# Kernel optimization log

Measured on AMD Instinct MI355X. Metric: run time of the kernel, lower is better.

## Reference

```python
import jax, jax.numpy as jnp
import numpy as np

DIM = 192
R = 16            # patches_resolution, D=H=W=R
SP = 4            # split_size
NH = 6            # num_heads (block level); per-branch heads = NH//3
B = 2
L = R * R * R
EPS = 1e-5


def layernorm(x, g, b):
    mu = jnp.mean(x, axis=-1, keepdims=True)
    var = jnp.mean(jnp.square(x - mu), axis=-1, keepdims=True)
    return (x - mu) * jax.lax.rsqrt(var + EPS) * g + b


def window_partition(x, d_sp, h_sp, w_sp, nh):
    b, _, _, _, cb = x.shape
    win = d_sp * h_sp * w_sp
    x = x.reshape(b, R // d_sp, d_sp, R // h_sp, h_sp, R // w_sp, w_sp, cb)
    x = x.transpose(0, 1, 3, 5, 2, 4, 6, 7).reshape(-1, win, nh, cb // nh)
    return x.transpose(0, 2, 1, 3)


def window_merge(x, d_sp, h_sp, w_sp, b):
    cb = x.shape[-1]
    x = x.reshape(b, R // d_sp, R // h_sp, R // w_sp, d_sp, h_sp, w_sp, cb)
    x = x.transpose(0, 1, 4, 2, 5, 3, 6, 7).reshape(b, L, cb)
    return x


def lepe_attention(q, k, v, d_sp, h_sp, w_sp, nh):
    # q,k,v: (B, L, Cb). Note: LePE bias is computed-but-unused in the source -> pure windowed SDPA.
    b, _, cb = q.shape
    hd = cb // nh
    scale = hd ** -0.5
    q5 = q.reshape(b, R, R, R, cb)
    k5 = k.reshape(b, R, R, R, cb)
    v5 = v.reshape(b, R, R, R, cb)
    qw = window_partition(q5, d_sp, h_sp, w_sp, nh) * scale
    kw = window_partition(k5, d_sp, h_sp, w_sp, nh)
    vw = window_partition(v5, d_sp, h_sp, w_sp, nh)
    attn = jax.nn.softmax(jnp.einsum('whqd,whkd->whqk', qw, kw), axis=-1)
    out = jnp.einsum('whqk,whkd->whqd', attn, vw)
    out = out.transpose(0, 2, 1, 3).reshape(-1, d_sp * h_sp * w_sp, cb)
    return window_merge(out, d_sp, h_sp, w_sp, b)


WINDOW_SHAPES = [(R, R, SP), (R, SP, R), (SP, R, R)]  # idx 0,1,2


def setup_inputs() -> dict:
    key = jax.random.key(0)
    ks = jax.random.split(key, 12)
    C = DIM
    H4 = int(C * 4)
    inp = {
        'x': jax.random.normal(ks[0], (B, C, R, R, R), dtype=jnp.float32),
        'w_qkv': jax.random.normal(ks[1], (C, 3 * C), dtype=jnp.float32) * (C ** -0.5),
        'w_proj': jax.random.normal(ks[2], (C, C), dtype=jnp.float32) * (C ** -0.5),
        'b_proj': jnp.zeros((C,), dtype=jnp.float32),
        'g1': jnp.ones((C,), dtype=jnp.float32),
        'b1': jnp.zeros((C,), dtype=jnp.float32),
        'g2': jnp.ones((C,), dtype=jnp.float32),
        'b2': jnp.zeros((C,), dtype=jnp.float32),
        'w_fc1': jax.random.normal(ks[3], (C, H4), dtype=jnp.float32) * (C ** -0.5),
        'b_fc1': jnp.zeros((H4,), dtype=jnp.float32),
        'w_fc2': jax.random.normal(ks[4], (H4, C), dtype=jnp.float32) * (H4 ** -0.5),
        'b_fc2': jnp.zeros((C,), dtype=jnp.float32),
    }
    return inp


def reference(x, w_qkv, w_proj, b_proj, g1, b1, g2, b2, w_fc1, b_fc1, w_fc2, b_fc2):
    C = DIM
    Cb = C // 3
    nh_b = NH // 3
    x = 2.0 * x
    xt = jnp.transpose(x, (0, 2, 3, 4, 1))                # (B, D, H, W, C)
    img = layernorm(xt, g1, b1)
    qkv = img.reshape(B, L, C) @ w_qkv                    # (B, L, 3C)
    q, k, v = jnp.split(qkv.reshape(B, L, 3, C).transpose(2, 0, 1, 3), 3, axis=0)
    q, k, v = q[0], k[0], v[0]                            # each (B, L, C)
    outs = []
    for i, (dsp, hsp, wsp) in enumerate(WINDOW_SHAPES):
        sl = slice(i * Cb, (i + 1) * Cb)
        outs.append(lepe_attention(q[..., sl], k[..., sl], v[..., sl], dsp, hsp, wsp, nh_b))
    attened = jnp.concatenate(outs, axis=2)               # (B, L, C)
    attened = attened @ w_proj + b_proj
    xs = xt.reshape(B, L, C) + attened
    h = layernorm(xs, g2, b2) @ w_fc1 + b_fc1
    h = jax.nn.gelu(h, approximate=False)
    xs = xs + (h @ w_fc2 + b_fc2)
    out = xs.reshape(B, R, R, R, C).transpose(0, 4, 1, 2, 3)  # (B, C, D, H, W)
    return out
```

## Files before the change

kernel.cpp:

```cpp
#include <hip/hip_runtime.h>
#include <hip/hip_bf16.h>

typedef __hip_bfloat16 bf16;
typedef short short8 __attribute__((ext_vector_type(8)));
typedef float floatx4 __attribute__((ext_vector_type(4)));

#define SZ (8192*192)

__device__ __forceinline__ unsigned short f2b(float f) {
    unsigned u = __builtin_bit_cast(unsigned, f);
    u += 0x7FFFu + ((u >> 16) & 1u);
    return (unsigned short)(u >> 16);
}
__device__ __forceinline__ float b2f(unsigned short h) {
    unsigned u = ((unsigned)h) << 16;
    return __builtin_bit_cast(float, u);
}
__device__ __forceinline__ unsigned pk2(float a, float b) {
    return ((unsigned)f2b(b) << 16) | (unsigned)f2b(a);
}

__global__ void detect_kernel(const unsigned short* __restrict__ x16, int* __restrict__ flag) {
    __shared__ int cnt;
    if (threadIdx.x == 0) cnt = 0;
    __syncthreads();
    int c = 0;
    for (int i = threadIdx.x; i < 8192; i += 256) {
        int e = (x16[i] >> 7) & 0xFF;
        if (e >= 152) c++;
    }
    if (c) atomicAdd(&cnt, c);
    __syncthreads();
    if (threadIdx.x == 0) *flag = (cnt >= 32) ? 1 : 0;
}

struct WPA { const void* s[11]; };

__global__ __launch_bounds__(256) void wprep_kernel(WPA a, unsigned short* __restrict__ wdst,
                                                    float* __restrict__ vdst,
                                                    const int* __restrict__ flag) {
    int i = blockIdx.x * 256 + threadIdx.x;
    int f = *flag;
    if (i < 442368) {
        int seg, base, K, N;
        if (i < 110592)      { seg = 0; base = 0;      K = 192; N = 576; }
        else if (i < 147456) { seg = 1; base = 110592; K = 192; N = 192; }
        else if (i < 294912) { seg = 2; base = 147456; K = 192; N = 768; }
        else                 { seg = 3; base = 294912; K = 768; N = 192; }
        int j = i - base;
        int n = j / K, k = j - n * K;
        size_t src = (size_t)k * N + n;
        float v = f ? ((const float*)a.s[seg])[src] : b2f(((const unsigned short*)a.s[seg])[src]);
        wdst[i] = f2b(v);
    } else if (i < 444288) {
        int j = i - 442368;
        int seg, off;
        if (j < 960)       { seg = 4 + j / 192; off = j % 192; }
        else if (j < 1728) { seg = 9; off = j - 960; }
        else               { seg = 10; off = j - 1728; }
        float v = f ? ((const float*)a.s[seg])[off] : b2f(((const unsigned short*)a.s[seg])[off]);
        vdst[j] = v;
    }
}

__global__ __launch_bounds__(256) void prep_kernel(const void* __restrict__ xin,
        const int* __restrict__ flag,
        const float* __restrict__ g1, const float* __restrict__ b1,
        float* __restrict__ xt, unsigned short* __restrict__ img) {
    __shared__ float tile[192][33];
    __shared__ float mu[32], rs[32];
    int tid = threadIdx.x;
    int t0 = blockIdx.x * 32;
    int b = t0 >> 12;
    int ts = t0 & 4095;
    int f = *flag;
    for (int idx = tid; idx < 192 * 32; idx += 256) {
        int c = idx >> 5, tt = idx & 31;
        int gi = ((b * 192 + c) << 12) + ts + tt;
        float raw = f ? ((const float*)xin)[gi] : b2f(((const unsigned short*)xin)[gi]);
        tile[c][tt] = 2.0f * raw;
    }
    __syncthreads();
    {
        int tt = tid >> 3, j = tid & 7;
        int c0 = j * 24;
        float s = 0.f, sq = 0.f;
        #pragma unroll
        for (int i = 0; i < 24; ++i) { float v = tile[c0 + i][tt]; s += v; sq += v * v; }
        s += __shfl_xor(s, 1); sq += __shfl_xor(sq, 1);
        s += __shfl_xor(s, 2); sq += __shfl_xor(sq, 2);
        s += __shfl_xor(s, 4); sq += __shfl_xor(sq, 4);
        if (j == 0) {
            float m = s * (1.0f / 192.0f);
            float var = sq * (1.0f / 192.0f) - m * m;
            mu[tt] = m;
            rs[tt] = rsqrtf(var + 1e-5f);
        }
    }
    __syncthreads();
    for (int idx = tid; idx < 32 * 192; idx += 256) {
        int tt = idx / 192, c = idx % 192;
        float v = tile[c][tt];
        int o = (t0 + tt) * 192 + c;
        xt[o] = v;
        img[o] = f2b((v - mu[tt]) * rs[tt] * g1[c] + b1[c]);
    }
}

template <int MODE, int W>
__global__ __launch_bounds__(64 * W) void mfma_gemm(const unsigned short* __restrict__ A,
        const unsigned short* __restrict__ WT, const float* __restrict__ bias,
        const float* __restrict__ resid, void* __restrict__ out, int N, int K) {
    int wave = threadIdx.x >> 6, lane = threadIdx.x & 63;
    int quad = lane >> 4, l16 = lane & 15;
    int m0 = blockIdx.x * (32 * W) + wave * 32, n0 = blockIdx.y * 64;
    const unsigned short* ap = A + (size_t)(m0 + l16) * K + quad * 8;
    const unsigned short* wp = WT + (size_t)(n0 + l16) * K + quad * 8;
    floatx4 acc[2][4] = {};
    #pragma unroll 2
    for (int kc = 0; kc < K; kc += 32) {
        short8 a0 = *reinterpret_cast<const short8*>(ap + kc);
        short8 a1 = *reinterpret_cast<const short8*>(ap + (size_t)16 * K + kc);
        #pragma unroll
        for (int nt = 0; nt < 4; ++nt) {
            short8 w = *reinterpret_cast<const short8*>(wp + (size_t)nt * 16 * K + kc);
            acc[0][nt] = __builtin_amdgcn_mfma_f32_16x16x32_bf16(a0, w, acc[0][nt], 0, 0, 0);
            acc[1][nt] = __builtin_amdgcn_mfma_f32_16x16x32_bf16(a1, w, acc[1][nt], 0, 0, 0);
        }
    }
    #pragma unroll
    for (int fh = 0; fh < 2; ++fh) {
        #pragma unroll
        for (int nt = 0; nt < 4; ++nt) {
            #pragma unroll
            for (int r = 0; r < 4; ++r) {
                int row = m0 + fh * 16 + quad * 4 + r;
                int col = n0 + nt * 16 + l16;
                float v = acc[fh][nt][r];
                if (MODE == 0 && col < 192) v *= 0.17677669529663689f;
                if (MODE >= 1) v += bias[col];
                if (MODE == 2) v = 0.5f * v * (1.0f + erff(v * 0.70710678118654752f));
                size_t o = (size_t)row * N + col;
                if (MODE == 0 || MODE == 2) ((unsigned short*)out)[o] = f2b(v);
                else                        ((float*)out)[o] = v + resid[o];
            }
        }
    }
}

__device__ __forceinline__ int tok_of(int br, int wb, int q) {
    if (br == 0) return ((q >> 6) << 8) | (((q >> 2) & 15) << 4) | (wb << 2) | (q & 3);
    else if (br == 1) return ((q >> 6) << 8) | (((wb << 2) + ((q >> 4) & 3)) << 4) | (q & 15);
    else return (((wb << 2) + (q >> 8)) << 8) | (q & 255);
}

__device__ __forceinline__ int vtaddr(int d) { return d * 72 + ((d >> 3) << 3); }

template <int SPLIT>
__global__ __launch_bounds__(256) void attn_mfma(const unsigned short* __restrict__ qkv,
        unsigned short* __restrict__ attb, float* __restrict__ po, float* __restrict__ pl) {
    __shared__ __align__(16) unsigned short P[4][16 * 72];
    __shared__ __align__(16) unsigned short VT[2][32 * 72 + 32];
    const int chunk = 96 * SPLIT;
    int hw = blockIdx.x;
    int bid = (hw & 7) * chunk + (hw >> 3);
    int kh, rest;
    if (SPLIT == 2) { kh = bid & 1; rest = bid >> 1; }
    else            { kh = 0;       rest = bid; }
    int qt = rest & 15, head = (rest >> 4) & 1, wb = (rest >> 5) & 3, b = (rest >> 7) & 1, br = rest >> 8;
    int tid = threadIdx.x;
    int wave = tid >> 6, lane = tid & 63, quad = lane >> 4, l16 = lane & 15;
    int coff = br * 64 + head * 32;
    int tb = b << 12;
    int tq = tok_of(br, wb, qt * 64 + wave * 16 + l16);
    short8 aq = *reinterpret_cast<const short8*>(qkv + (size_t)(tb + tq) * 576 + coff + quad * 8);
    floatx4 o0 = {}, o1 = {};
    float lsum[4] = {0.f, 0.f, 0.f, 0.f};
    unsigned short* Pw = P[wave];
    int vkey5 = lane >> 2;
    int vd = lane & 3;
    int vcol = 4 * vkey5 + wave;

    const int NT = 16 / SPLIT;
    const int kt0 = kh * NT;
    const int kc0 = kt0 * 64;
    const size_t stp = (size_t)((br == 2) ? 64 : 256) * 576;

    const unsigned short* vp  = qkv + (size_t)(tb + tok_of(br, wb, kc0 + wave * 16 + vkey5)) * 576 + 384 + coff + vd * 8;
    const unsigned short* kpA = qkv + (size_t)(tb + tok_of(br, wb, kc0 + l16))      * 576 + 192 + coff + quad * 8;
    const unsigned short* kpB = qkv + (size_t)(tb + tok_of(br, wb, kc0 + 16 + l16)) * 576 + 192 + coff + quad * 8;
    const unsigned short* kpC = qkv + (size_t)(tb + tok_of(br, wb, kc0 + 32 + l16)) * 576 + 192 + coff + quad * 8;
    const unsigned short* kpD = qkv + (size_t)(tb + tok_of(br, wb, kc0 + 48 + l16)) * 576 + 192 + coff + quad * 8;

    short8 vv = *reinterpret_cast<const short8*>(vp);
    short8 k0 = *reinterpret_cast<const short8*>(kpA);
    short8 k1 = *reinterpret_cast<const short8*>(kpB);
    short8 k2 = *reinterpret_cast<const short8*>(kpC);
    short8 k3 = *reinterpret_cast<const short8*>(kpD);

    for (int it = 0; it < NT; ++it) {
        unsigned short* VTb = VT[it & 1];
        #pragma unroll
        for (int j = 0; j < 8; ++j)
            VTb[vtaddr(vd * 8 + j) + vcol] = (unsigned short)vv[j];
        short8 ck0 = k0, ck1 = k1, ck2 = k2, ck3 = k3;
        if (it + 1 < NT) {
            vp += stp; kpA += stp; kpB += stp; kpC += stp; kpD += stp;
            vv = *reinterpret_cast<const short8*>(vp);
            k0 = *reinterpret_cast<const short8*>(kpA);
            k1 = *reinterpret_cast<const short8*>(kpB);
            k2 = *reinterpret_cast<const short8*>(kpC);
            k3 = *reinterpret_cast<const short8*>(kpD);
        }
        __syncthreads();
        floatx4 z = {};
        floatx4 s0 = __builtin_amdgcn_mfma_f32_16x16x32_bf16(aq, ck0, z, 0, 0, 0);
        floatx4 s1 = __builtin_amdgcn_mfma_f32_16x16x32_bf16(aq, ck1, z, 0, 0, 0);
        floatx4 s2 = __builtin_amdgcn_mfma_f32_16x16x32_bf16(aq, ck2, z, 0, 0, 0);
        floatx4 s3 = __builtin_amdgcn_mfma_f32_16x16x32_bf16(aq, ck3, z, 0, 0, 0);
        #pragma unroll
        for (int r = 0; r < 4; ++r) {
            float p0 = __expf(s0[r]);
            float p1 = __expf(s1[r]);
            float p2 = __expf(s2[r]);
            float p3 = __expf(s3[r]);
            lsum[r] += (p0 + p1) + (p2 + p3);
            uint2 w2; w2.x = pk2(p0, p1); w2.y = pk2(p2, p3);
            *reinterpret_cast<uint2*>(Pw + (quad * 4 + r) * 72 + 4 * l16) = w2;
        }
        const unsigned short* pr = Pw + l16 * 72;
        short8 a0 = *reinterpret_cast<const short8*>(pr + quad * 8);
        short8 a1 = *reinterpret_cast<const short8*>(pr + 32 + quad * 8);
        const unsigned short* v0r = VTb + vtaddr(l16);
        const unsigned short* v1r = VTb + vtaddr(16 + l16);
        short8 b00 = *reinterpret_cast<const short8*>(v0r + quad * 8);
        short8 b01 = *reinterpret_cast<const short8*>(v0r + 32 + quad * 8);
        short8 b10 = *reinterpret_cast<const short8*>(v1r + quad * 8);
        short8 b11 = *reinterpret_cast<const short8*>(v1r + 32 + quad * 8);
        o0 = __builtin_amdgcn_mfma_f32_16x16x32_bf16(a0, b00, o0, 0, 0, 0);
        o0 = __builtin_amdgcn_mfma_f32_16x16x32_bf16(a1, b01, o0, 0, 0, 0);
        o1 = __builtin_amdgcn_mfma_f32_16x16x32_bf16(a0, b10, o1, 0, 0, 0);
        o1 = __builtin_amdgcn_mfma_f32_16x16x32_bf16(a1, b11, o1, 0, 0, 0);
    }
    #pragma unroll
    for (int r = 0; r < 4; ++r) {
        float ls = lsum[r];
        ls += __shfl_xor(ls, 1);
        ls += __shfl_xor(ls, 2);
        ls += __shfl_xor(ls, 4);
        ls += __shfl_xor(ls, 8);
        lsum[r] = ls;
    }
    if (SPLIT == 2) {
        #pragma unroll
        for (int r = 0; r < 4; ++r) {
            int q = qt * 64 + wave * 16 + quad * 4 + r;
            int t = tok_of(br, wb, q);
            size_t o = ((size_t)(kh << 13) + tb + t) * 192 + coff;
            po[o + l16]      = o0[r];
            po[o + 16 + l16] = o1[r];
            if (l16 == 0) pl[(size_t)((kh << 13) + tb + t) * 6 + br * 2 + head] = lsum[r];
        }
    } else {
        #pragma unroll
        for (int r = 0; r < 4; ++r) {
            float inv = 1.0f / lsum[r];
            int q = qt * 64 + wave * 16 + quad * 4 + r;
            int t = tok_of(br, wb, q);
            size_t o = (size_t)(tb + t) * 192 + coff;
            attb[o + l16]      = f2b(o0[r] * inv);
            attb[o + 16 + l16] = f2b(o1[r] * inv);
        }
    }
}

__global__ __launch_bounds__(256) void attn_combine(const float* __restrict__ po,
        const float* __restrict__ pl, unsigned short* __restrict__ attb) {
    int token = (blockIdx.x << 2) + (threadIdx.x >> 6);
    int lane = threadIdx.x & 63;
    const float* r0 = po + (size_t)token * 192;
    const float* r1 = r0 + (size_t)8192 * 192;
    const float* q0 = pl + (size_t)token * 6;
    const float* q1 = q0 + (size_t)8192 * 6;
    unsigned short* orow = attb + (size_t)token * 192;
    #pragma unroll
    for (int sgm = 0; sgm < 3; ++sgm) {
        int d = lane + sgm * 64;
        int g = d >> 5;
        float denom = q0[g] + q1[g];
        orow[d] = f2b((r0[d] + r1[d]) / denom);
    }
}

__global__ __launch_bounds__(256) void ln_kernel(const float* __restrict__ in,
        const float* __restrict__ g, const float* __restrict__ bb, unsigned short* __restrict__ out) {
    int token = (blockIdx.x << 2) + (threadIdx.x >> 6);
    int lane = threadIdx.x & 63;
    const float* row = in + (size_t)token * 192;
    float v0 = row[lane], v1 = row[lane + 64], v2 = row[lane + 128];
    float s = v0 + v1 + v2, sq = v0 * v0 + v1 * v1 + v2 * v2;
    #pragma unroll
    for (int mask = 1; mask < 64; mask <<= 1) {
        s += __shfl_xor(s, mask);
        sq += __shfl_xor(sq, mask);
    }
    float m = s * (1.f / 192.f);
    float var = sq * (1.f / 192.f) - m * m;
    float rsd = rsqrtf(var + 1e-5f);
    unsigned short* orow = out + (size_t)token * 192;
    orow[lane]       = f2b((v0 - m) * rsd * g[lane]       + bb[lane]);
    orow[lane + 64]  = f2b((v1 - m) * rsd * g[lane + 64]  + bb[lane + 64]);
    orow[lane + 128] = f2b((v2 - m) * rsd * g[lane + 128] + bb[lane + 128]);
}

__global__ __launch_bounds__(256) void unprep_kernel(const float* __restrict__ xs,
                                                     void* __restrict__ out,
                                                     const int* __restrict__ flag) {
    __shared__ float tile[192][33];
    int tid = threadIdx.x;
    int t0 = blockIdx.x * 32;
    int b = t0 >> 12, ts = t0 & 4095;
    for (int idx = tid; idx < 32 * 192; idx += 256) {
        int tt = idx / 192, c = idx % 192;
        tile[c][tt] = xs[(size_t)(t0 + tt) * 192 + c];
    }
    __syncthreads();
    int f = *flag;
    for (int idx = tid; idx < 192 * 32; idx += 256) {
        int c = idx >> 5, tt = idx & 31;
        float v = tile[c][tt];
        int o = ((b * 192 + c) << 12) + ts + tt;
        if (f) ((float*)out)[o] = v;
        else   ((unsigned short*)out)[o] = f2b(v);
    }
}

extern "C" void kernel_launch(void* const* d_in, const int* in_sizes, int n_in,
                              void* d_out, int out_size, void* d_ws, size_t ws_size,
                              hipStream_t stream) {
    float* ws = (float*)d_ws;

    float* vbase = ws;
    float* bprojf = vbase + 0;
    float* g1f    = vbase + 192;
    float* b1f    = vbase + 384;
    float* g2f    = vbase + 576;
    float* b2f    = vbase + 768;
    float* bfc1f  = vbase + 960;
    float* bfc2f  = vbase + 1728;

    unsigned short* wbase = (unsigned short*)(ws + 1920);
    unsigned short* wqkvT = wbase + 0;
    unsigned short* wprojT = wbase + 110592;
    unsigned short* wfc1T = wbase + 147456;
    unsigned short* wfc2T = wbase + 294912;

    size_t p = 1920 + 442368 / 2;
    float* xt = ws + p; p += SZ;
    unsigned short* img = (unsigned short*)(ws + p); p += SZ / 2;
    size_t pQ = p;
    unsigned short* qkv = (unsigned short*)(ws + pQ);
    unsigned short* hbuf = (unsigned short*)(ws + pQ);
    p = pQ + 8192 * 768 / 2;
    unsigned short* attb = (unsigned short*)(ws + p); p += SZ / 2;
    int* flag = (int*)(ws + p); p += 16;
    float* po = ws + p; p += (size_t)2 * 8192 * 192;
    float* pl = ws + p; p += (size_t)2 * 8192 * 6;
    bool split_ok = ws_size >= p * sizeof(float);
    float* xs = xt;
    unsigned short* lnb = img;

    WPA wa;
    wa.s[0] = d_in[1];  wa.s[1] = d_in[2];  wa.s[2] = d_in[8];  wa.s[3] = d_in[10];
    wa.s[4] = d_in[3];  wa.s[5] = d_in[4];  wa.s[6] = d_in[5];  wa.s[7] = d_in[6];
    wa.s[8] = d_in[7];  wa.s[9] = d_in[9];  wa.s[10] = d_in[11];

    detect_kernel<<<dim3(1), dim3(256), 0, stream>>>((const unsigned short*)d_in[0], flag);
    wprep_kernel<<<dim3(1736), dim3(256), 0, stream>>>(wa, wbase, vbase, flag);
    prep_kernel<<<dim3(256), dim3(256), 0, stream>>>(d_in[0], flag, g1f, b1f, xt, img);
    mfma_gemm<0, 2><<<dim3(128, 9), dim3(128), 0, stream>>>(
        img, wqkvT, nullptr, nullptr, qkv, 576, 192);
    if (split_ok) {
        attn_mfma<2><<<dim3(1536), dim3(256), 0, stream>>>(qkv, nullptr, po, pl);
        attn_combine<<<dim3(2048), dim3(256), 0, stream>>>(po, pl, attb);
    } else {
        attn_mfma<1><<<dim3(768), dim3(256), 0, stream>>>(qkv, attb, nullptr, nullptr);
    }
    mfma_gemm<1, 1><<<dim3(256, 3), dim3(64), 0, stream>>>(
        attb, wprojT, bprojf, xt, xs, 192, 192);
    ln_kernel<<<dim3(2048), dim3(256), 0, stream>>>(xs, g2f, b2f, lnb);
    mfma_gemm<2, 2><<<dim3(128, 12), dim3(128), 0, stream>>>(
        lnb, wfc1T, bfc1f, nullptr, hbuf, 768, 192);
    mfma_gemm<3, 1><<<dim3(256, 3), dim3(64), 0, stream>>>(
        hbuf, wfc2T, bfc2f, xs, xs, 192, 768);
    unprep_kernel<<<dim3(256), dim3(256), 0, stream>>>(xs, d_out, flag);
}
```

Baseline: 206.1 us.

## Write V pre-transposed from QKV GEMM epilogue and drop LDS V staging

The QKV GEMM epilogue now writes the V columns into a separate buffer that is transposed and permuted per branch/head/window, matching the MFMA B-operand layout. The attention kernel loads V fragments directly from global memory instead of staging V through a double-buffered LDS transpose, and it drops the per-iteration __syncthreads. The aim is to remove LDS transpose stores and the block barrier from the attention loop. In exchange the GEMM epilogue does scattered 2-byte strided stores, the workspace grows, and the K/V register prefetch across iterations is gone.

```diff
diff --git a/kernel.cpp b/kernel.cpp
--- a/kernel.cpp
+++ b/kernel.cpp
@@ -107,10 +107,17 @@
     }
 }
 
+__device__ __forceinline__ int g_of(int br, int t) {
+    if (br == 0) return (((t >> 2) & 3) << 10) | ((t >> 8) << 6) | (((t >> 4) & 15) << 2) | (t & 3);
+    if (br == 1) return (((t >> 6) & 3) << 10) | ((t >> 8) << 6) | (((t >> 4) & 3) << 4) | (t & 15);
+    return t;
+}
+
 template <int MODE, int W>
 __global__ __launch_bounds__(64 * W) void mfma_gemm(const unsigned short* __restrict__ A,
         const unsigned short* __restrict__ WT, const float* __restrict__ bias,
-        const float* __restrict__ resid, void* __restrict__ out, int N, int K) {
+        const float* __restrict__ resid, void* __restrict__ out,
+        unsigned short* __restrict__ vt, int N, int K) {
     int wave = threadIdx.x >> 6, lane = threadIdx.x & 63;
     int quad = lane >> 4, l16 = lane & 15;
     int m0 = blockIdx.x * (32 * W) + wave * 32, n0 = blockIdx.y * 64;
@@ -132,17 +139,30 @@
     for (int fh = 0; fh < 2; ++fh) {
         #pragma unroll
         for (int nt = 0; nt < 4; ++nt) {
-            #pragma unroll
-            for (int r = 0; r < 4; ++r) {
-                int row = m0 + fh * 16 + quad * 4 + r;
-                int col = n0 + nt * 16 + l16;
-                float v = acc[fh][nt][r];
-                if (MODE == 0 && col < 192) v *= 0.17677669529663689f;
-                if (MODE >= 1) v += bias[col];
-                if (MODE == 2) v = 0.5f * v * (1.0f + erff(v * 0.70710678118654752f));
-                size_t o = (size_t)row * N + col;
-                if (MODE == 0 || MODE == 2) ((unsigned short*)out)[o] = f2b(v);
-                else                        ((float*)out)[o] = v + resid[o];
+            int col = n0 + nt * 16 + l16;
+            if (MODE == 0 && n0 >= 384) {
+                int cv = col - 384;
+                int row0 = m0 + fh * 16 + quad * 4;
+                int bb_ = row0 >> 12, tl = row0 & 4095;
+                int g0 = g_of(cv >> 6, tl);
+                int pp = (g0 & ~63) + 4 * (g0 & 15) + ((g0 >> 4) & 3);
+                unsigned short* vrow = vt + ((size_t)((bb_ * 6 + (cv >> 5)) * 32 + (cv & 31)) << 12);
+                vrow[pp]      = f2b(acc[fh][nt][0]);
+                vrow[pp + 4]  = f2b(acc[fh][nt][1]);
+                vrow[pp + 8]  = f2b(acc[fh][nt][2]);
+                vrow[pp + 12] = f2b(acc[fh][nt][3]);
+            } else {
+                #pragma unroll
+                for (int r = 0; r < 4; ++r) {
+                    int row = m0 + fh * 16 + quad * 4 + r;
+                    float v = acc[fh][nt][r];
+                    if (MODE == 0 && col < 192) v *= 0.17677669529663689f;
+                    if (MODE >= 1) v += bias[col];
+                    if (MODE == 2) v = 0.5f * v * (1.0f + erff(v * 0.70710678118654752f));
+                    size_t o = (size_t)row * N + col;
+                    if (MODE == 0 || MODE == 2) ((unsigned short*)out)[o] = f2b(v);
+                    else                        ((float*)out)[o] = v + resid[o];
+                }
             }
         }
     }
@@ -154,13 +174,11 @@
     else return (((wb << 2) + (q >> 8)) << 8) | (q & 255);
 }
 
-__device__ __forceinline__ int vtaddr(int d) { return d * 72 + ((d >> 3) << 3); }
-
 template <int SPLIT>
 __global__ __launch_bounds__(256) void attn_mfma(const unsigned short* __restrict__ qkv,
+        const unsigned short* __restrict__ vt,
         unsigned short* __restrict__ attb, float* __restrict__ po, float* __restrict__ pl) {
     __shared__ __align__(16) unsigned short P[4][16 * 72];
-    __shared__ __align__(16) unsigned short VT[2][32 * 72 + 32];
     const int chunk = 96 * SPLIT;
     int hw = blockIdx.x;
     int bid = (hw & 7) * chunk + (hw >> 3);
@@ -177,47 +195,35 @@
     floatx4 o0 = {}, o1 = {};
     float lsum[4] = {0.f, 0.f, 0.f, 0.f};
     unsigned short* Pw = P[wave];
-    int vkey5 = lane >> 2;
-    int vd = lane & 3;
-    int vcol = 4 * vkey5 + wave;
 
     const int NT = 16 / SPLIT;
-    const int kt0 = kh * NT;
-    const int kc0 = kt0 * 64;
+    const int kc0 = kh * NT * 64;
     const size_t stp = (size_t)((br == 2) ? 64 : 256) * 576;
 
-    const unsigned short* vp  = qkv + (size_t)(tb + tok_of(br, wb, kc0 + wave * 16 + vkey5)) * 576 + 384 + coff + vd * 8;
     const unsigned short* kpA = qkv + (size_t)(tb + tok_of(br, wb, kc0 + l16))      * 576 + 192 + coff + quad * 8;
     const unsigned short* kpB = qkv + (size_t)(tb + tok_of(br, wb, kc0 + 16 + l16)) * 576 + 192 + coff + quad * 8;
     const unsigned short* kpC = qkv + (size_t)(tb + tok_of(br, wb, kc0 + 32 + l16)) * 576 + 192 + coff + quad * 8;
     const unsigned short* kpD = qkv + (size_t)(tb + tok_of(br, wb, kc0 + 48 + l16)) * 576 + 192 + coff + quad * 8;
-
-    short8 vv = *reinterpret_cast<const short8*>(vp);
-    short8 k0 = *reinterpret_cast<const short8*>(kpA);
-    short8 k1 = *reinterpret_cast<const short8*>(kpB);
-    short8 k2 = *reinterpret_cast<const short8*>(kpC);
-    short8 k3 = *reinterpret_cast<const short8*>(kpD);
+    const unsigned short* vsl = vt + ((size_t)((b * 6 + br * 2 + head) * 32) << 12) + (wb << 10) + kc0 + quad * 8;
+    const unsigned short* v0p = vsl + ((size_t)l16 << 12);
+    const unsigned short* v1p = vsl + ((size_t)(l16 + 16) << 12);
 
     for (int it = 0; it < NT; ++it) {
-        unsigned short* VTb = VT[it & 1];
-        #pragma unroll
-        for (int j = 0; j < 8; ++j)
-            VTb[vtaddr(vd * 8 + j) + vcol] = (unsigned short)vv[j];
-        short8 ck0 = k0, ck1 = k1, ck2 = k2, ck3 = k3;
-        if (it + 1 < NT) {
-            vp += stp; kpA += stp; kpB += stp; kpC += stp; kpD += stp;
-            vv = *reinterpret_cast<const short8*>(vp);
-            k0 = *reinterpret_cast<const short8*>(kpA);
-            k1 = *reinterpret_cast<const short8*>(kpB);
-            k2 = *reinterpret_cast<const short8*>(kpC);
-            k3 = *reinterpret_cast<const short8*>(kpD);
-        }
-        __syncthreads();
+        short8 k0 = *reinterpret_cast<const short8*>(kpA);
+        short8 k1 = *reinterpret_cast<const short8*>(kpB);
+        short8 k2 = *reinterpret_cast<const short8*>(kpC);
+        short8 k3 = *reinterpret_cast<const short8*>(kpD);
+        short8 vb00 = *reinterpret_cast<const short8*>(v0p);
+        short8 vb01 = *reinterpret_cast<const short8*>(v0p + 32);
+        short8 vb10 = *reinterpret_cast<const short8*>(v1p);
+        short8 vb11 = *reinterpret_cast<const short8*>(v1p + 32);
+        kpA += stp; kpB += stp; kpC += stp; kpD += stp;
+        v0p += 64; v1p += 64;
         floatx4 z = {};
-        floatx4 s0 = __builtin_amdgcn_mfma_f32_16x16x32_bf16(aq, ck0, z, 0, 0, 0);
-        floatx4 s1 = __builtin_amdgcn_mfma_f32_16x16x32_bf16(aq, ck1, z, 0, 0, 0);
-        floatx4 s2 = __builtin_amdgcn_mfma_f32_16x16x32_bf16(aq, ck2, z, 0, 0, 0);
-        floatx4 s3 = __builtin_amdgcn_mfma_f32_16x16x32_bf16(aq, ck3, z, 0, 0, 0);
+        floatx4 s0 = __builtin_amdgcn_mfma_f32_16x16x32_bf16(aq, k0, z, 0, 0, 0);
+        floatx4 s1 = __builtin_amdgcn_mfma_f32_16x16x32_bf16(aq, k1, z, 0, 0, 0);
+        floatx4 s2 = __builtin_amdgcn_mfma_f32_16x16x32_bf16(aq, k2, z, 0, 0, 0);
+        floatx4 s3 = __builtin_amdgcn_mfma_f32_16x16x32_bf16(aq, k3, z, 0, 0, 0);
         #pragma unroll
         for (int r = 0; r < 4; ++r) {
             float p0 = __expf(s0[r]);
@@ -231,16 +237,10 @@
         const unsigned short* pr = Pw + l16 * 72;
         short8 a0 = *reinterpret_cast<const short8*>(pr + quad * 8);
         short8 a1 = *reinterpret_cast<const short8*>(pr + 32 + quad * 8);
-        const unsigned short* v0r = VTb + vtaddr(l16);
-        const unsigned short* v1r = VTb + vtaddr(16 + l16);
-        short8 b00 = *reinterpret_cast<const short8*>(v0r + quad * 8);
-        short8 b01 = *reinterpret_cast<const short8*>(v0r + 32 + quad * 8);
-        short8 b10 = *reinterpret_cast<const short8*>(v1r + quad * 8);
-        short8 b11 = *reinterpret_cast<const short8*>(v1r + 32 + quad * 8);
-        o0 = __builtin_amdgcn_mfma_f32_16x16x32_bf16(a0, b00, o0, 0, 0, 0);
-        o0 = __builtin_amdgcn_mfma_f32_16x16x32_bf16(a1, b01, o0, 0, 0, 0);
-        o1 = __builtin_amdgcn_mfma_f32_16x16x32_bf16(a0, b10, o1, 0, 0, 0);
-        o1 = __builtin_amdgcn_mfma_f32_16x16x32_bf16(a1, b11, o1, 0, 0, 0);
+        o0 = __builtin_amdgcn_mfma_f32_16x16x32_bf16(a0, vb00, o0, 0, 0, 0);
+        o0 = __builtin_amdgcn_mfma_f32_16x16x32_bf16(a1, vb01, o0, 0, 0, 0);
+        o1 = __builtin_amdgcn_mfma_f32_16x16x32_bf16(a0, vb10, o1, 0, 0, 0);
+        o1 = __builtin_amdgcn_mfma_f32_16x16x32_bf16(a1, vb11, o1, 0, 0, 0);
     }
     #pragma unroll
     for (int r = 0; r < 4; ++r) {
@@ -364,6 +364,7 @@
     p = pQ + 8192 * 768 / 2;
     unsigned short* attb = (unsigned short*)(ws + p); p += SZ / 2;
     int* flag = (int*)(ws + p); p += 16;
+    unsigned short* vtb = (unsigned short*)(ws + p); p += SZ / 2;
     float* po = ws + p; p += (size_t)2 * 8192 * 192;
     float* pl = ws + p; p += (size_t)2 * 8192 * 6;
     bool split_ok = ws_size >= p * sizeof(float);
@@ -379,19 +380,19 @@
     wprep_kernel<<<dim3(1736), dim3(256), 0, stream>>>(wa, wbase, vbase, flag);
     prep_kernel<<<dim3(256), dim3(256), 0, stream>>>(d_in[0], flag, g1f, b1f, xt, img);
     mfma_gemm<0, 2><<<dim3(128, 9), dim3(128), 0, stream>>>(
-        img, wqkvT, nullptr, nullptr, qkv, 576, 192);
+        img, wqkvT, nullptr, nullptr, qkv, vtb, 576, 192);
     if (split_ok) {
-        attn_mfma<2><<<dim3(1536), dim3(256), 0, stream>>>(qkv, nullptr, po, pl);
+        attn_mfma<2><<<dim3(1536), dim3(256), 0, stream>>>(qkv, vtb, nullptr, po, pl);
         attn_combine<<<dim3(2048), dim3(256), 0, stream>>>(po, pl, attb);
     } else {
-        attn_mfma<1><<<dim3(768), dim3(256), 0, stream>>>(qkv, attb, nullptr, nullptr);
+        attn_mfma<1><<<dim3(768), dim3(256), 0, stream>>>(qkv, vtb, attb, nullptr, nullptr);
     }
     mfma_gemm<1, 1><<<dim3(256, 3), dim3(64), 0, stream>>>(
-        attb, wprojT, bprojf, xt, xs, 192, 192);
+        attb, wprojT, bprojf, xt, xs, nullptr, 192, 192);
     ln_kernel<<<dim3(2048), dim3(256), 0, stream>>>(xs, g2f, b2f, lnb);
     mfma_gemm<2, 2><<<dim3(128, 12), dim3(128), 0, stream>>>(
-        lnb, wfc1T, bfc1f, nullptr, hbuf, 768, 192);
+        lnb, wfc1T, bfc1f, nullptr, hbuf, nullptr, 768, 192);
     mfma_gemm<3, 1><<<dim3(256, 3), dim3(64), 0, stream>>>(
-        hbuf, wfc2T, bfc2f, xs, xs, 192, 768);
+        hbuf, wfc2T, bfc2f, xs, xs, nullptr, 192, 768);
     unprep_kernel<<<dim3(256), dim3(256), 0, stream>>>(xs, d_out, flag);
 }
```

Measured after the change: 225.0 us. +9.2%, slower.
